# Kernel optimization log

Hardware: AMD Instinct MI355X
Metric: run time of the kernel (lower is better)

## Reference

```python
import jax, jax.numpy as jnp
import numpy as np

EMB = 768
HEADS = 8


def setup_inputs() -> dict:
    key = jax.random.key(0)
    ks = jax.random.split(key, 5)
    b, n, e = 4, 2048, EMB
    x = jax.random.normal(ks[0], (b, n, e), dtype=jnp.float32)
    Wqkv = jax.random.normal(ks[1], (e, 3 * e), dtype=jnp.float32) * (e ** -0.5)
    bqkv = jax.random.normal(ks[2], (3 * e,), dtype=jnp.float32) * 0.02
    Wproj = jax.random.normal(ks[3], (e, e), dtype=jnp.float32) * (e ** -0.5)
    bproj = jax.random.normal(ks[4], (e,), dtype=jnp.float32) * 0.02
    return {"x": x, "Wqkv": Wqkv, "bqkv": bqkv, "Wproj": Wproj, "bproj": bproj}


def reference(x, Wqkv, bqkv, Wproj, bproj):
    b, n, e = x.shape
    h = HEADS
    d = e // h
    # fused qkv projection; rearrange 'b n (h d qkv) -> qkv b h n d'
    # NOTE: qkv is the innermost factor of the last dim in the original einops pattern.
    qkv = (x @ Wqkv + bqkv).reshape(b, n, h, d, 3)  # [b, n, h, d, 3]
    q = jnp.transpose(qkv[..., 0], (0, 2, 1, 3))  # [b, h, n, d]
    k = jnp.transpose(qkv[..., 1], (0, 2, 1, 3))
    v = jnp.transpose(qkv[..., 2], (0, 2, 1, 3))
    # NOTE: the original scales by sqrt(emb_size), not sqrt(head_dim).
    scale = jnp.float32(e) ** 0.5
    energy = jnp.einsum('bhqd,bhkd->bhqk', q, k)  # full O(n^2) score matrix
    attn = jax.nn.softmax(energy / scale, axis=-1)  # dropout p=0 -> identity
    out = jnp.einsum('bhqk,bhkd->bhqd', attn, v)
    out = jnp.transpose(out, (0, 2, 1, 3)).reshape(b, n, e)  # b h n d -> b n (h d)
    return out @ Wproj + bproj
```

## Files before the change

kernel.cpp:

```cpp
#include <hip/hip_runtime.h>
#include <hip/hip_bf16.h>
#include <stdint.h>

#define EMB   768
#define HEADS 8
#define HDIM  96
#define SEQ   2048
#define BATCH 4
#define MROWS (BATCH*SEQ)

typedef unsigned short ushort_t;
typedef __bf16 bf16x8 __attribute__((ext_vector_type(8)));
typedef float  fx4    __attribute__((ext_vector_type(4)));
typedef uint4  uint4_a  __attribute__((may_alias));
typedef uint2  uint2_a  __attribute__((may_alias));
typedef bf16x8 bf16x8_a __attribute__((may_alias));

__device__ __forceinline__ float bf2f(ushort_t u) {
    uint32_t v = ((uint32_t)u) << 16;
    return __builtin_bit_cast(float, v);
}
__device__ __forceinline__ ushort_t f2bf(float f) {
    uint32_t u = __builtin_bit_cast(uint32_t, f);
    u += 0x7fffu + ((u >> 16) & 1u);
    return (ushort_t)(u >> 16);
}
__device__ __forceinline__ uint32_t pk2(float a, float b) {
    __hip_bfloat162 h = __float22bfloat162_rn(make_float2(a, b));
    uint32_t r;
    __builtin_memcpy(&r, &h, 4);
    return r;
}
__device__ __forceinline__ void load_lds16(const void* g, void* l) {
    __builtin_amdgcn_global_load_lds(
        (const __attribute__((address_space(1))) uint32_t*)g,
        (__attribute__((address_space(3))) uint32_t*)l, 16, 0, 0);
}

__global__ __launch_bounds__(256) void detect_f32(const uint32_t* __restrict__ x,
                                                  int* __restrict__ flag) {
    __shared__ int cnt;
    if (threadIdx.x == 0) cnt = 0;
    __syncthreads();
    int local = 0;
    for (int i = threadIdx.x; i < 4096; i += 256) {
        uint32_t e = (x[i] >> 7) & 0xFFu;
        local += (e >= 64u && e <= 143u) ? 1 : 0;
    }
    atomicAdd(&cnt, local);
    __syncthreads();
    if (threadIdx.x == 0) *flag = (cnt < 3500) ? 1 : 0;
}

__global__ __launch_bounds__(256) void transpose_conv(
        const void* __restrict__ vsrc, ushort_t* __restrict__ dst,
        int R, int C, const int* __restrict__ flag)
{
    __shared__ __attribute__((aligned(16))) ushort_t tile[64][72];
    const int c0 = blockIdx.x * 64, r0 = blockIdx.y * 64;
    const int t = threadIdx.x;
    const int isf32 = *flag;
#pragma unroll
    for (int i = 0; i < 2; ++i) {
        int idx = i * 256 + t;
        int r = idx >> 3, c8 = (idx & 7) * 8;
        if (isf32) {
            const float* s = (const float*)vsrc + (size_t)(r0 + r) * C + c0 + c8;
            float4 v0 = *(const float4*)s, v1 = *(const float4*)(s + 4);
            uint32_t tmp[4] = { pk2(v0.x, v0.y), pk2(v0.z, v0.w),
                                pk2(v1.x, v1.y), pk2(v1.z, v1.w) };
            *(uint4_a*)&tile[r][c8] = *(const uint4_a*)tmp;
        } else {
            const ushort_t* s = (const ushort_t*)vsrc + (size_t)(r0 + r) * C + c0 + c8;
            *(uint4_a*)&tile[r][c8] = *(const uint4_a*)s;
        }
    }
    __syncthreads();
#pragma unroll
    for (int i = 0; i < 2; ++i) {
        int idx = i * 256 + t;
        int r = idx >> 3, k8 = (idx & 7) * 8;
        ushort_t tmp[8];
#pragma unroll
        for (int j = 0; j < 8; ++j) tmp[j] = tile[k8 + j][r];
        *(uint4_a*)&dst[(size_t)(c0 + r) * R + r0 + k8] = *(const uint4_a*)tmp;
    }
}

__global__ __launch_bounds__(256, 2) void qkv_mfma(
        const void* __restrict__ x, const ushort_t* __restrict__ Wt1,
        const void* __restrict__ bias,
        ushort_t* __restrict__ stage, int u0, const int* __restrict__ flag)
{
    __shared__ __attribute__((aligned(16))) ushort_t lA[128 * 32];
    __shared__ __attribute__((aligned(16))) ushort_t lB[96 * 32];
    const int g = blockIdx.z, u = u0 + g;
    const int b = u >> 3, h = u & 7;
    const int m0 = blockIdx.x * 128;
    const int n0 = blockIdx.y * 96;
    const bool isf = (*flag != 0);
    const int t = threadIdx.x, lane = t & 63, wave = t >> 6;
    const int lx = lane & 15, quad = lane >> 4;
    const int wm = (wave & 1) * 64, wn = (wave >> 1) * 48;
    const int hb = h * 288;
    const size_t xrow0 = (size_t)(b * SEQ + m0) * EMB;
    const float qscale = 0.03608439182435161f;

    ushort_t* Qg = stage + (size_t)g * (3 * SEQ * HDIM);
    ushort_t* Kg = Qg + SEQ * HDIM;
    ushort_t* Vg = Qg + 2 * SEQ * HDIM;

    fx4 acc[4][3] = {};

    for (int kt = 0; kt < EMB / 32; ++kt) {
        const int k0 = kt * 32;
        __syncthreads();
        if (isf) {
            const float* xf = (const float*)x;
#pragma unroll
            for (int it = 0; it < 4; ++it) {
                int idx = it * 256 + t;
                int r = idx >> 3, k4 = (idx & 7) * 4;
                float4 v = *(const float4*)&xf[xrow0 + (size_t)r * EMB + k0 + k4];
                uint32_t tmp[2] = { pk2(v.x, v.y), pk2(v.z, v.w) };
                *(uint2_a*)&lA[r * 32 + k4] = *(const uint2_a*)tmp;
            }
        } else {
            const ushort_t* xb = (const ushort_t*)x;
#pragma unroll
            for (int it = 0; it < 2; ++it) {
                int idx = it * 256 + t;
                int r = idx >> 2, k8 = (idx & 3) * 8;
                *(uint4_a*)&lA[r * 32 + k8] = *(const uint4_a*)&xb[xrow0 + (size_t)r * EMB + k0 + k8];
            }
        }
        {
            int c = t >> 2, s8 = (t & 3) * 8;
            load_lds16(&Wt1[(size_t)(hb + n0 + c) * EMB + k0 + s8], &lB[t * 8]);
            if (t < 128) {
                int idx = 256 + t;
                int c2 = idx >> 2, s82 = (idx & 3) * 8;
                load_lds16(&Wt1[(size_t)(hb + n0 + c2) * EMB + k0 + s82], &lB[idx * 8]);
            }
        }
        __syncthreads();

        bf16x8 af[4], bfr[3];
#pragma unroll
        for (int i = 0; i < 4; ++i)
            af[i] = *(const bf16x8_a*)&lA[(wm + i * 16 + lx) * 32 + quad * 8];
#pragma unroll
        for (int j = 0; j < 3; ++j)
            bfr[j] = *(const bf16x8_a*)&lB[(wn + j * 16 + lx) * 32 + quad * 8];
#pragma unroll
        for (int i = 0; i < 4; ++i)
#pragma unroll
            for (int j = 0; j < 3; ++j)
                acc[i][j] = __builtin_amdgcn_mfma_f32_16x16x32_bf16(af[i], bfr[j], acc[i][j], 0, 0, 0);
    }

#pragma unroll
    for (int j = 0; j < 3; ++j) {
        const int cl = n0 + wn + j * 16 + lx;
        const int dd = cl / 3, s = cl - dd * 3;
        const float bv = isf ? ((const float*)bias)[hb + cl]
                             : bf2f(((const ushort_t*)bias)[hb + cl]);
#pragma unroll
        for (int i = 0; i < 4; ++i) {
            const int ml = m0 + wm + i * 16 + quad * 4;
#pragma unroll
            for (int r = 0; r < 4; ++r) {
                const int nseq = ml + r;
                const float v = acc[i][j][r] + bv;
                if (s == 0)      Qg[(size_t)nseq * HDIM + dd] = f2bf(v * qscale);
                else if (s == 1) Kg[(size_t)nseq * HDIM + dd] = f2bf(v);
                else             Vg[(size_t)dd * SEQ + nseq] = f2bf(v);
            }
        }
    }
}

__global__ __launch_bounds__(256, 2) void attn_flash(
        const ushort_t* __restrict__ stage, ushort_t* __restrict__ O, int u0)
{
    __shared__ __attribute__((aligned(16))) ushort_t lQ[64 * 104];
    __shared__ __attribute__((aligned(16))) ushort_t lK[64 * 104];
    __shared__ __attribute__((aligned(16))) ushort_t lV[96 * 72];
    __shared__ __attribute__((aligned(16))) ushort_t lP[4][16 * 72];
    const int t = threadIdx.x, lane = t & 63, wave = t >> 6;
    const int lx = lane & 15, quad = lane >> 4;
    const int qt = blockIdx.x, g = blockIdx.y, u = u0 + g;
    const int b = u >> 3, h = u & 7;
    const ushort_t* Qb = stage + (size_t)g * (3 * SEQ * HDIM);
    const ushort_t* Kb = Qb + SEQ * HDIM;
    const ushort_t* Vb = Qb + 2 * SEQ * HDIM;

#pragma unroll
    for (int it = 0; it < 3; ++it) {
        int idx = it * 256 + t;
        int r = idx / 12, s8 = (idx % 12) * 8;
        *(uint4_a*)&lQ[r * 104 + s8] = *(const uint4_a*)&Qb[(size_t)(qt * 64 + r) * HDIM + s8];
    }

    fx4 accO[6] = {};
    float lsum[4] = {0.f, 0.f, 0.f, 0.f};

    for (int kt = 0; kt < SEQ / 64; ++kt) {
        __syncthreads();
#pragma unroll
        for (int it = 0; it < 3; ++it) {
            int idx = it * 256 + t;
            { int r = idx / 12, s8 = (idx % 12) * 8;
              *(uint4_a*)&lK[r * 104 + s8] = *(const uint4_a*)&Kb[(size_t)(kt * 64 + r) * HDIM + s8]; }
            { int r = idx >> 3, s8 = (idx & 7) * 8;
              *(uint4_a*)&lV[r * 72 + s8] = *(const uint4_a*)&Vb[(size_t)r * SEQ + kt * 64 + s8]; }
        }
        __syncthreads();

        fx4 accS[4] = {};
#pragma unroll
        for (int kd = 0; kd < 3; ++kd) {
            bf16x8 aq = *(const bf16x8_a*)&lQ[(wave * 16 + lx) * 104 + kd * 32 + quad * 8];
#pragma unroll
            for (int j = 0; j < 4; ++j) {
                bf16x8 bk = *(const bf16x8_a*)&lK[(j * 16 + lx) * 104 + kd * 32 + quad * 8];
                accS[j] = __builtin_amdgcn_mfma_f32_16x16x32_bf16(aq, bk, accS[j], 0, 0, 0);
            }
        }

#pragma unroll
        for (int r = 0; r < 4; ++r) {
#pragma unroll
            for (int j = 0; j < 4; ++j) {
                float p = __expf(accS[j][r]);
                lsum[r] += p;
                lP[wave][(quad * 4 + r) * 72 + j * 16 + lx] = f2bf(p);
            }
        }
        asm volatile("s_waitcnt lgkmcnt(0)" ::: "memory");

#pragma unroll
        for (int kk = 0; kk < 2; ++kk) {
            bf16x8 ap = *(const bf16x8_a*)&lP[wave][lx * 72 + kk * 32 + quad * 8];
#pragma unroll
            for (int d = 0; d < 6; ++d) {
                bf16x8 bv = *(const bf16x8_a*)&lV[(d * 16 + lx) * 72 + kk * 32 + quad * 8];
                accO[d] = __builtin_amdgcn_mfma_f32_16x16x32_bf16(ap, bv, accO[d], 0, 0, 0);
            }
        }
    }

#pragma unroll
    for (int r = 0; r < 4; ++r) {
        float s = lsum[r];
#pragma unroll
        for (int off = 1; off < 16; off <<= 1) s += __shfl_xor(s, off, 64);
        const float inv = 1.0f / s;
        const int nseq = qt * 64 + wave * 16 + quad * 4 + r;
        ushort_t* orow = O + ((size_t)(b * SEQ + nseq)) * EMB + h * HDIM;
#pragma unroll
        for (int d = 0; d < 6; ++d)
            orow[d * 16 + lx] = f2bf(accO[d][r] * inv);
    }
}

__global__ __launch_bounds__(256, 2) void proj_gemm(
        const ushort_t* __restrict__ A, const ushort_t* __restrict__ Wt2,
        const void* __restrict__ bias, float* __restrict__ out,
        const int* __restrict__ flag)
{
    constexpr int KDIM = EMB;
    __shared__ __attribute__((aligned(16))) ushort_t lA[128 * 32];
    __shared__ __attribute__((aligned(16))) ushort_t lB[128 * 32];
    const int t = threadIdx.x;
    const int m0 = blockIdx.x * 128, n0 = blockIdx.y * 128;
    const bool isf = (*flag != 0);
    const int lane = t & 63, wave = t >> 6;
    const int wm = (wave & 1) * 64, wn = (wave >> 1) * 64;
    const int lx = lane & 15, quad = lane >> 4;

    fx4 acc[4][4] = {};

    for (int kt = 0; kt < KDIM / 32; ++kt) {
        const int k0 = kt * 32;
        __syncthreads();
#pragma unroll
        for (int it = 0; it < 2; ++it) {
            int idx = it * 256 + t;
            int r = idx >> 2, s8 = (idx & 3) * 8;
            load_lds16(&A  [(size_t)(m0 + r) * KDIM + k0 + s8], &lA[idx * 8]);
            load_lds16(&Wt2[(size_t)(n0 + r) * KDIM + k0 + s8], &lB[idx * 8]);
        }
        __syncthreads();

        bf16x8 af[4], bfr[4];
#pragma unroll
        for (int i = 0; i < 4; ++i)
            af[i] = *(const bf16x8_a*)&lA[(wm + i * 16 + lx) * 32 + quad * 8];
#pragma unroll
        for (int j = 0; j < 4; ++j)
            bfr[j] = *(const bf16x8_a*)&lB[(wn + j * 16 + lx) * 32 + quad * 8];
#pragma unroll
        for (int i = 0; i < 4; ++i)
#pragma unroll
            for (int j = 0; j < 4; ++j)
                acc[i][j] = __builtin_amdgcn_mfma_f32_16x16x32_bf16(af[i], bfr[j], acc[i][j], 0, 0, 0);
    }

#pragma unroll
    for (int j = 0; j < 4; ++j) {
        const int c = n0 + wn + j * 16 + lx;
        const float bv = isf ? ((const float*)bias)[c] : bf2f(((const ushort_t*)bias)[c]);
#pragma unroll
        for (int i = 0; i < 4; ++i) {
            const int mr = m0 + wm + i * 16 + quad * 4;
#pragma unroll
            for (int r = 0; r < 4; ++r)
                out[(size_t)(mr + r) * EMB + c] = acc[i][j][r] + bv;
        }
    }
}

extern "C" void kernel_launch(void* const* d_in, const int* in_sizes, int n_in,
                              void* d_out, int out_size, void* d_ws, size_t ws_size,
                              hipStream_t stream) {
    const void* x     = d_in[0];
    const void* Wqkv  = d_in[1];
    const void* bqkv  = d_in[2];
    const void* Wproj = d_in[3];
    const void* bproj = d_in[4];
    float* out = (float*)d_out;

    char* ws = (char*)d_ws;
    int* flag = (int*)ws;
    size_t off = 1024;
    ushort_t* Ob  = (ushort_t*)(ws + off);  off += (size_t)MROWS * EMB * 2;
    ushort_t* Wt1 = (ushort_t*)(ws + off);  off += (size_t)2304 * EMB * 2;
    ushort_t* Wt2 = (ushort_t*)(ws + off);  off += (size_t)EMB * EMB * 2;
    ushort_t* stage = (ushort_t*)(ws + off);
    const size_t SLOT_BYTES = (size_t)3 * SEQ * HDIM * 2;
    size_t avail = ws_size > off ? ws_size - off : 0;
    int G = (int)(avail / SLOT_BYTES);
    if (G < 1) G = 1;
    if (G > 32) G = 32;

    detect_f32<<<1, 256, 0, stream>>>((const uint32_t*)x, flag);
    transpose_conv<<<dim3(2304 / 64, EMB / 64), 256, 0, stream>>>(Wqkv, Wt1, EMB, 2304, flag);
    transpose_conv<<<dim3(EMB / 64, EMB / 64), 256, 0, stream>>>(Wproj, Wt2, EMB, EMB, flag);
    for (int u0 = 0; u0 < 32; u0 += G) {
        const int gc = (32 - u0 < G) ? (32 - u0) : G;
        qkv_mfma<<<dim3(16, 3, gc), 256, 0, stream>>>(x, Wt1, bqkv, stage, u0, flag);
        attn_flash<<<dim3(SEQ / 64, gc), 256, 0, stream>>>(stage, Ob, u0);
    }
    proj_gemm<<<dim3(MROWS / 128, EMB / 128), 256, 0, stream>>>(Ob, Wt2, bproj, out, flag);
}
```

Before: 315.7 us.

## Pre-convert x to bf16 once and double query rows per attention block

A new pre-pass converts x to bf16 into a workspace buffer once. The QKV GEMM then streams the A tile straight into LDS with global_load_lds instead of converting fp32 to bf16 in registers on every one of the 8 head passes. The attention kernel now handles 128 query rows per block, with each wave doing two 16-row sub-tiles, so every K/V tile loaded into LDS serves twice as many queries and the V fragments are hoisted into registers. In exchange it halves the attention grid, raises register and LDS use per block, and adds an extra full pass over x plus workspace memory.

```diff
diff --git a/kernel.cpp b/kernel.cpp
--- a/kernel.cpp
+++ b/kernel.cpp
@@ -50,6 +50,19 @@
     atomicAdd(&cnt, local);
     __syncthreads();
     if (threadIdx.x == 0) *flag = (cnt < 3500) ? 1 : 0;
+}
+
+__global__ __launch_bounds__(256) void canon_x(const void* __restrict__ src,
+        ushort_t* __restrict__ dst, const int* __restrict__ flag) {
+    const int i = (blockIdx.x * 256 + threadIdx.x) * 8;
+    if (*flag) {
+        const float* s = (const float*)src + i;
+        float4 a = *(const float4*)s, b = *(const float4*)(s + 4);
+        uint32_t tmp[4] = { pk2(a.x, a.y), pk2(a.z, a.w), pk2(b.x, b.y), pk2(b.z, b.w) };
+        *(uint4_a*)&dst[i] = *(const uint4_a*)tmp;
+    } else {
+        *(uint4_a*)&dst[i] = *(const uint4_a*)((const ushort_t*)src + i);
+    }
 }
 
 __global__ __launch_bounds__(256) void transpose_conv(
@@ -88,7 +101,7 @@
 }
 
 __global__ __launch_bounds__(256, 2) void qkv_mfma(
-        const void* __restrict__ x, const ushort_t* __restrict__ Wt1,
+        const ushort_t* __restrict__ Xc, const ushort_t* __restrict__ Wt1,
         const void* __restrict__ bias,
         ushort_t* __restrict__ stage, int u0, const int* __restrict__ flag)
 {
@@ -115,24 +128,11 @@
     for (int kt = 0; kt < EMB / 32; ++kt) {
         const int k0 = kt * 32;
         __syncthreads();
-        if (isf) {
-            const float* xf = (const float*)x;
-#pragma unroll
-            for (int it = 0; it < 4; ++it) {
-                int idx = it * 256 + t;
-                int r = idx >> 3, k4 = (idx & 7) * 4;
-                float4 v = *(const float4*)&xf[xrow0 + (size_t)r * EMB + k0 + k4];
-                uint32_t tmp[2] = { pk2(v.x, v.y), pk2(v.z, v.w) };
-                *(uint2_a*)&lA[r * 32 + k4] = *(const uint2_a*)tmp;
-            }
-        } else {
-            const ushort_t* xb = (const ushort_t*)x;
-#pragma unroll
-            for (int it = 0; it < 2; ++it) {
-                int idx = it * 256 + t;
-                int r = idx >> 2, k8 = (idx & 3) * 8;
-                *(uint4_a*)&lA[r * 32 + k8] = *(const uint4_a*)&xb[xrow0 + (size_t)r * EMB + k0 + k8];
-            }
+#pragma unroll
+        for (int it = 0; it < 2; ++it) {
+            int idx = it * 256 + t;
+            int r = idx >> 2, k8 = (idx & 3) * 8;
+            load_lds16(&Xc[xrow0 + (size_t)r * EMB + k0 + k8], &lA[idx * 8]);
         }
         {
             int c = t >> 2, s8 = (t & 3) * 8;
@@ -183,7 +183,7 @@
 __global__ __launch_bounds__(256, 2) void attn_flash(
         const ushort_t* __restrict__ stage, ushort_t* __restrict__ O, int u0)
 {
-    __shared__ __attribute__((aligned(16))) ushort_t lQ[64 * 104];
+    __shared__ __attribute__((aligned(16))) ushort_t lQ[128 * 104];
     __shared__ __attribute__((aligned(16))) ushort_t lK[64 * 104];
     __shared__ __attribute__((aligned(16))) ushort_t lV[96 * 72];
     __shared__ __attribute__((aligned(16))) ushort_t lP[4][16 * 72];
@@ -196,14 +196,14 @@
     const ushort_t* Vb = Qb + 2 * SEQ * HDIM;
 
 #pragma unroll
-    for (int it = 0; it < 3; ++it) {
+    for (int it = 0; it < 6; ++it) {
         int idx = it * 256 + t;
         int r = idx / 12, s8 = (idx % 12) * 8;
-        *(uint4_a*)&lQ[r * 104 + s8] = *(const uint4_a*)&Qb[(size_t)(qt * 64 + r) * HDIM + s8];
-    }
-
-    fx4 accO[6] = {};
-    float lsum[4] = {0.f, 0.f, 0.f, 0.f};
+        *(uint4_a*)&lQ[r * 104 + s8] = *(const uint4_a*)&Qb[(size_t)(qt * 128 + r) * HDIM + s8];
+    }
+
+    fx4 accO[2][6] = {};
+    float lsum[2][4] = {};
 
     for (int kt = 0; kt < SEQ / 64; ++kt) {
         __syncthreads();
@@ -217,50 +217,62 @@
         }
         __syncthreads();
 
-        fx4 accS[4] = {};
+        fx4 accS[2][4] = {};
 #pragma unroll
         for (int kd = 0; kd < 3; ++kd) {
-            bf16x8 aq = *(const bf16x8_a*)&lQ[(wave * 16 + lx) * 104 + kd * 32 + quad * 8];
+            bf16x8 aq0 = *(const bf16x8_a*)&lQ[(wave * 32 + lx) * 104 + kd * 32 + quad * 8];
+            bf16x8 aq1 = *(const bf16x8_a*)&lQ[(wave * 32 + 16 + lx) * 104 + kd * 32 + quad * 8];
 #pragma unroll
             for (int j = 0; j < 4; ++j) {
                 bf16x8 bk = *(const bf16x8_a*)&lK[(j * 16 + lx) * 104 + kd * 32 + quad * 8];
-                accS[j] = __builtin_amdgcn_mfma_f32_16x16x32_bf16(aq, bk, accS[j], 0, 0, 0);
-            }
-        }
-
+                accS[0][j] = __builtin_amdgcn_mfma_f32_16x16x32_bf16(aq0, bk, accS[0][j], 0, 0, 0);
+                accS[1][j] = __builtin_amdgcn_mfma_f32_16x16x32_bf16(aq1, bk, accS[1][j], 0, 0, 0);
+            }
+        }
+
+        bf16x8 bv[2][6];
+#pragma unroll
+        for (int kk = 0; kk < 2; ++kk)
+#pragma unroll
+            for (int d = 0; d < 6; ++d)
+                bv[kk][d] = *(const bf16x8_a*)&lV[(d * 16 + lx) * 72 + kk * 32 + quad * 8];
+
+#pragma unroll
+        for (int i = 0; i < 2; ++i) {
+#pragma unroll
+            for (int r = 0; r < 4; ++r) {
+#pragma unroll
+                for (int j = 0; j < 4; ++j) {
+                    float p = __expf(accS[i][j][r]);
+                    lsum[i][r] += p;
+                    lP[wave][(quad * 4 + r) * 72 + j * 16 + lx] = f2bf(p);
+                }
+            }
+            asm volatile("s_waitcnt lgkmcnt(0)" ::: "memory");
+#pragma unroll
+            for (int kk = 0; kk < 2; ++kk) {
+                bf16x8 ap = *(const bf16x8_a*)&lP[wave][lx * 72 + kk * 32 + quad * 8];
+#pragma unroll
+                for (int d = 0; d < 6; ++d)
+                    accO[i][d] = __builtin_amdgcn_mfma_f32_16x16x32_bf16(ap, bv[kk][d], accO[i][d], 0, 0, 0);
+            }
+        }
+    }
+
+#pragma unroll
+    for (int i = 0; i < 2; ++i) {
 #pragma unroll
         for (int r = 0; r < 4; ++r) {
-#pragma unroll
-            for (int j = 0; j < 4; ++j) {
-                float p = __expf(accS[j][r]);
-                lsum[r] += p;
-                lP[wave][(quad * 4 + r) * 72 + j * 16 + lx] = f2bf(p);
-            }
-        }
-        asm volatile("s_waitcnt lgkmcnt(0)" ::: "memory");
-
-#pragma unroll
-        for (int kk = 0; kk < 2; ++kk) {
-            bf16x8 ap = *(const bf16x8_a*)&lP[wave][lx * 72 + kk * 32 + quad * 8];
-#pragma unroll
-            for (int d = 0; d < 6; ++d) {
-                bf16x8 bv = *(const bf16x8_a*)&lV[(d * 16 + lx) * 72 + kk * 32 + quad * 8];
-                accO[d] = __builtin_amdgcn_mfma_f32_16x16x32_bf16(ap, bv, accO[d], 0, 0, 0);
-            }
-        }
-    }
-
-#pragma unroll
-    for (int r = 0; r < 4; ++r) {
-        float s = lsum[r];
-#pragma unroll
-        for (int off = 1; off < 16; off <<= 1) s += __shfl_xor(s, off, 64);
-        const float inv = 1.0f / s;
-        const int nseq = qt * 64 + wave * 16 + quad * 4 + r;
-        ushort_t* orow = O + ((size_t)(b * SEQ + nseq)) * EMB + h * HDIM;
-#pragma unroll
-        for (int d = 0; d < 6; ++d)
-            orow[d * 16 + lx] = f2bf(accO[d][r] * inv);
+            float s = lsum[i][r];
+#pragma unroll
+            for (int off = 1; off < 16; off <<= 1) s += __shfl_xor(s, off, 64);
+            const float inv = 1.0f / s;
+            const int nseq = qt * 128 + wave * 32 + i * 16 + quad * 4 + r;
+            ushort_t* orow = O + ((size_t)(b * SEQ + nseq)) * EMB + h * HDIM;
+#pragma unroll
+            for (int d = 0; d < 6; ++d)
+                orow[d * 16 + lx] = f2bf(accO[i][d][r] * inv);
+        }
     }
 }
 
@@ -335,6 +347,7 @@
     int* flag = (int*)ws;
     size_t off = 1024;
     ushort_t* Ob  = (ushort_t*)(ws + off);  off += (size_t)MROWS * EMB * 2;
+    ushort_t* Xc  = (ushort_t*)(ws + off);  off += (size_t)MROWS * EMB * 2;
     ushort_t* Wt1 = (ushort_t*)(ws + off);  off += (size_t)2304 * EMB * 2;
     ushort_t* Wt2 = (ushort_t*)(ws + off);  off += (size_t)EMB * EMB * 2;
     ushort_t* stage = (ushort_t*)(ws + off);
@@ -345,12 +358,13 @@
     if (G > 32) G = 32;
 
     detect_f32<<<1, 256, 0, stream>>>((const uint32_t*)x, flag);
+    canon_x<<<dim3(MROWS * EMB / (256 * 8)), 256, 0, stream>>>(x, Xc, flag);
     transpose_conv<<<dim3(2304 / 64, EMB / 64), 256, 0, stream>>>(Wqkv, Wt1, EMB, 2304, flag);
     transpose_conv<<<dim3(EMB / 64, EMB / 64), 256, 0, stream>>>(Wproj, Wt2, EMB, EMB, flag);
     for (int u0 = 0; u0 < 32; u0 += G) {
         const int gc = (32 - u0 < G) ? (32 - u0) : G;
-        qkv_mfma<<<dim3(16, 3, gc), 256, 0, stream>>>(x, Wt1, bqkv, stage, u0, flag);
-        attn_flash<<<dim3(SEQ / 64, gc), 256, 0, stream>>>(stage, Ob, u0);
+        qkv_mfma<<<dim3(16, 3, gc), 256, 0, stream>>>(Xc, Wt1, bqkv, stage, u0, flag);
+        attn_flash<<<dim3(SEQ / 128, gc), 256, 0, stream>>>(stage, Ob, u0);
     }
     proj_gemm<<<dim3(MROWS / 128, EMB / 128), 256, 0, stream>>>(Ob, Wt2, bproj, out, flag);
 }
```

Result: faster. 261.0 us (-17.3%).
